# Kernel optimization log

Hardware: AMD Instinct MI355X
Metric: run time of the kernel (lower is better)

The kernel has to match this reference:

```python
import jax, jax.numpy as jnp
import numpy as np

P = 3          # graph partitions
CO = 64        # out_channels
KS = 9         # temporal kernel size (Gamma)
STRIDE = 1     # temporal stride
EPS = 1e-3     # keras BatchNormalization default epsilon


def setup_inputs() -> dict:
    key = jax.random.key(0)
    k1, k2, k3 = jax.random.split(key, 3)
    x = jax.random.normal(k1, (32, 64, 300, 25), dtype=jnp.float32)      # (N, C_in, L, V)
    A = jax.random.uniform(k2, (3, 25, 25), dtype=jnp.float32)           # (P, V, V)
    W = jax.random.normal(k3, (64, 192), dtype=jnp.float32) * 0.05       # (C_in, C_out*P)
    gamma = jnp.ones((64,), dtype=jnp.float32)
    beta = jnp.zeros((64,), dtype=jnp.float32)
    mean = jnp.zeros((64,), dtype=jnp.float32)
    var = jnp.ones((64,), dtype=jnp.float32)
    return {"x": x, "A": A, "W": W, "gamma": gamma, "beta": beta, "mean": mean, "var": var}


def _lt_matrix(L):
    # sum of shifted identities: lt[r, r + i*STRIDE] = 1 for i in [0, KS//STRIDE)
    lt = jnp.zeros((L, L), dtype=jnp.float32)
    for i in range(KS // STRIDE):
        lt = lt + jnp.eye(L, k=i * STRIDE, dtype=jnp.float32)
    return lt


def reference(x, A, W, gamma, beta, mean, var):
    N, C, L, V = x.shape
    res = x  # identity residual (in_channels == out_channels, stride == 1)
    # 1x1 conv: (N,C,L,V) x (C, CO*P) -> (N, CO*P, L, V); channel k = c*P + p (split into CO groups of P)
    y = jnp.einsum('nclv,ck->nklv', x, W)
    y = y.reshape(N, CO, P, L, V)  # (N, C_out, P, L, V)
    # partitioned graph matmul over joints: contract V with A[p]
    z = jnp.einsum('ncplv,pvw->ncplw', y, A)
    # temporal aggregation via handcrafted banded matrix, then sum over partitions
    lt = _lt_matrix(L)
    t = jnp.einsum('ncplv,lm->ncmv', z, lt)  # partition sum fused into einsum
    # BN (inference) over channel axis + ReLU
    inv = gamma / jnp.sqrt(var + EPS)
    xn = (t - mean[None, :, None, None]) * inv[None, :, None, None] + beta[None, :, None, None]
    xn = jax.nn.relu(xn)
    # residual add + final ReLU (dropout is identity at inference)
    return jax.nn.relu(xn + res)
```

## Files before the change

kernel.cpp:

```cpp
#include <hip/hip_runtime.h>
#include <cstdint>
#include <cstddef>

typedef short bf16x8 __attribute__((ext_vector_type(8)));
typedef float f32x4 __attribute__((ext_vector_type(4)));

#define EPS 1e-3f

__device__ __forceinline__ unsigned short f32_to_bf16(float f) {
    union { float f; uint32_t u; } v; v.f = f;
    uint32_t u = v.u;
    return (unsigned short)((u + 0x7FFFu + ((u >> 16) & 1u)) >> 16);
}

__global__ __launch_bounds__(256) void prep_kernel(const float* __restrict__ A,
                                                   const float* __restrict__ W,
                                                   unsigned short* __restrict__ wt,
                                                   unsigned short* __restrict__ at) {
    int idx = blockIdx.x * 256 + threadIdx.x;
    if (idx < 12288) {
        int kp = idx >> 6, ci = idx & 63;
        wt[idx] = f32_to_bf16(W[ci * 192 + kp]);
    } else {
        int j = idx - 12288;
        if (j < 3072) {
            int w = j / 96, k = j - w * 96;
            float val = 0.f;
            if (w < 25 && k < 75) {
                int p = k / 25, v = k - p * 25;
                val = A[(p * 25 + v) * 25 + w];
            }
            at[j] = f32_to_bf16(val);
        }
    }
}

__global__ __launch_bounds__(256) void window_kernel(const float* __restrict__ x,
                                                     unsigned short* __restrict__ xw) {
    int ci = blockIdx.x, n = blockIdx.y;
    __shared__ float sl[7500];
    const float4* xp4 = (const float4*)(x + (size_t)(n * 64 + ci) * 7500);
    float4* sl4 = (float4*)sl;
    for (int i = threadIdx.x; i < 1875; i += 256) sl4[i] = xp4[i];
    __syncthreads();
    unsigned short* base = xw + (size_t)n * 491520 + ci * 256;
    for (int i = threadIdx.x; i < 3840; i += 256) {
        int ch = i >> 7;
        int col = (i & 127) << 1;
        int e0 = ch * 250 + col;
        ushort2 r;
        #pragma unroll
        for (int h = 0; h < 2; ++h) {
            int e = e0 + h;
            float t = 0.f;
            if (e < 7500) {
                int m = e / 25, w = e - m * 25;
                int lo = m - 8 > 0 ? m - 8 : 0;
                for (int l = lo; l <= m; ++l) t += sl[l * 25 + w];
            }
            unsigned short b = f32_to_bf16(t);
            if (h == 0) r.x = b; else r.y = b;
        }
        *(ushort2*)(base + ch * 16384 + col) = r;
    }
}

__global__ __launch_bounds__(256, 2) void fused_kernel(
    const unsigned short* __restrict__ xw, const unsigned short* __restrict__ wt,
    const unsigned short* __restrict__ at, const float* __restrict__ x,
    const float* __restrict__ gamma, const float* __restrict__ beta,
    const float* __restrict__ mean, const float* __restrict__ var,
    float* __restrict__ out) {
    int chunk = blockIdx.x;
    int n = blockIdx.y;
    int l0 = chunk * 10;
    int tid = threadIdx.x;
    int wv = tid >> 6, lane = tid & 63, q = lane >> 4, lcol = lane & 15;

    __shared__ unsigned short Ys[160 * 104];
    __shared__ float scs[64], shs[64];

    if (tid < 64) {
        float sc = gamma[tid] * rsqrtf(var[tid] + EPS);
        scs[tid] = sc;
        shs[tid] = beta[tid] - mean[tid] * sc;
    }
    for (int i = tid; i < 5120; i += 256) {
        int r = i >> 5, j = 72 + (i & 31);
        Ys[r * 104 + j] = 0;
    }

    const unsigned short* xwb = xw + (size_t)n * 491520 + chunk * 16384;
    bf16x8 b1[4][2];
    #pragma unroll
    for (int nt = 0; nt < 4; ++nt) {
        #pragma unroll
        for (int s = 0; s < 2; ++s) {
            const unsigned short* p = xwb + (32 * s + 8 * q) * 256 + wv * 64 + nt * 16 + lcol;
            bf16x8 f;
            #pragma unroll
            for (int j = 0; j < 8; ++j) f[j] = (short)p[j * 256];
            b1[nt][s] = f;
        }
    }
    bf16x8 b2[2][3];
    #pragma unroll
    for (int nt = 0; nt < 2; ++nt)
        #pragma unroll
        for (int s = 0; s < 3; ++s)
            b2[nt][s] = *(const bf16x8*)(at + (nt * 16 + lcol) * 96 + 32 * s + 8 * q);

    for (int g = 0; g < 4; ++g) {
        f32x4 acc[3][4];
        #pragma unroll
        for (int mt = 0; mt < 3; ++mt)
            #pragma unroll
            for (int nt = 0; nt < 4; ++nt) acc[mt][nt] = (f32x4){0.f, 0.f, 0.f, 0.f};
        #pragma unroll
        for (int s = 0; s < 2; ++s) {
            #pragma unroll
            for (int mt = 0; mt < 3; ++mt) {
                bf16x8 a1 = *(const bf16x8*)(wt + (g * 48 + mt * 16 + lcol) * 64 + 32 * s + 8 * q);
                #pragma unroll
                for (int nt = 0; nt < 4; ++nt)
                    acc[mt][nt] = __builtin_amdgcn_mfma_f32_16x16x32_bf16(a1, b1[nt][s], acc[mt][nt], 0, 0, 0);
            }
        }
        __syncthreads();
        #pragma unroll
        for (int mt = 0; mt < 3; ++mt) {
            #pragma unroll
            for (int nt = 0; nt < 4; ++nt) {
                int col = wv * 64 + nt * 16 + lcol;
                if (col < 250) {
                    int ll = col / 25, v = col - ll * 25;
                    int rowbase = ll * 16;
                    #pragma unroll
                    for (int r = 0; r < 4; ++r) {
                        int kp = mt * 16 + 4 * q + r;
                        int cl = kp / 3, p = kp - cl * 3;
                        Ys[(rowbase + cl) * 104 + p * 25 + v] = f32_to_bf16(acc[mt][nt][r]);
                    }
                }
            }
        }
        __syncthreads();
        for (int l = wv; l < 10; l += 4) {
            f32x4 c0 = {0.f, 0.f, 0.f, 0.f}, c1 = {0.f, 0.f, 0.f, 0.f};
            #pragma unroll
            for (int s = 0; s < 3; ++s) {
                bf16x8 a2 = *(const bf16x8*)&Ys[(l * 16 + lcol) * 104 + 32 * s + 8 * q];
                c0 = __builtin_amdgcn_mfma_f32_16x16x32_bf16(a2, b2[0][s], c0, 0, 0, 0);
                c1 = __builtin_amdgcn_mfma_f32_16x16x32_bf16(a2, b2[1][s], c1, 0, 0, 0);
            }
            #pragma unroll
            for (int nt = 0; nt < 2; ++nt) {
                int w = nt * 16 + lcol;
                if (w < 25) {
                    f32x4 cc = nt ? c1 : c0;
                    #pragma unroll
                    for (int r = 0; r < 4; ++r) {
                        int c = g * 16 + 4 * q + r;
                        size_t gi = ((size_t)(n * 64 + c) * 300 + (l0 + l)) * 25 + w;
                        float o = fmaxf(cc[r] * scs[c] + shs[c], 0.f);
                        out[gi] = fmaxf(o + x[gi], 0.f);
                    }
                }
            }
        }
    }
}

extern "C" void kernel_launch(void* const* d_in, const int* in_sizes, int n_in,
                              void* d_out, int out_size, void* d_ws, size_t ws_size,
                              hipStream_t stream) {
    const float* x     = (const float*)d_in[0];
    const float* A     = (const float*)d_in[1];
    const float* W     = (const float*)d_in[2];
    const float* gamma = (const float*)d_in[3];
    const float* beta  = (const float*)d_in[4];
    const float* mean  = (const float*)d_in[5];
    const float* var   = (const float*)d_in[6];
    float* out = (float*)d_out;

    char* ws = (char*)d_ws;
    unsigned short* wt = (unsigned short*)ws;
    unsigned short* at = (unsigned short*)(ws + 24576);
    unsigned short* xw = (unsigned short*)(ws + 30720);

    prep_kernel<<<60, 256, 0, stream>>>(A, W, wt, at);
    window_kernel<<<dim3(64, 32), 256, 0, stream>>>(x, xw);
    fused_kernel<<<dim3(30, 32), 256, 0, stream>>>(xw, wt, at, x, gamma, beta, mean, var, out);
}
```

Before: 186.3 us.

## Fuse temporal window sum into main kernel, removing intermediate bf16 buffer

Removes the separate window kernel and its global bf16 intermediate. Each block now computes the 9-tap sliding temporal sum for its 10-timestep chunk directly from x with a running sum and stages it in shared memory in an MFMA-friendly layout. The block grows to 512 threads, so each wave handles half as many columns. This saves one launch and a global write+read round trip, at the cost of strided uncoalesced reads of x with an 8-step halo overlap per chunk.

```diff
diff --git a/kernel.cpp b/kernel.cpp
--- a/kernel.cpp
+++ b/kernel.cpp
@@ -7,10 +7,10 @@
 
 #define EPS 1e-3f
 
-__device__ __forceinline__ unsigned short f32_to_bf16(float f) {
+__device__ __forceinline__ short f32_to_bf16s(float f) {
     union { float f; uint32_t u; } v; v.f = f;
     uint32_t u = v.u;
-    return (unsigned short)((u + 0x7FFFu + ((u >> 16) & 1u)) >> 16);
+    return (short)((u + 0x7FFFu + ((u >> 16) & 1u)) >> 16);
 }
 
 __global__ __launch_bounds__(256) void prep_kernel(const float* __restrict__ A,
@@ -20,7 +20,7 @@
     int idx = blockIdx.x * 256 + threadIdx.x;
     if (idx < 12288) {
         int kp = idx >> 6, ci = idx & 63;
-        wt[idx] = f32_to_bf16(W[ci * 192 + kp]);
+        wt[idx] = (unsigned short)f32_to_bf16s(W[ci * 192 + kp]);
     } else {
         int j = idx - 12288;
         if (j < 3072) {
@@ -30,54 +30,24 @@
                 int p = k / 25, v = k - p * 25;
                 val = A[(p * 25 + v) * 25 + w];
             }
-            at[j] = f32_to_bf16(val);
+            at[j] = (unsigned short)f32_to_bf16s(val);
         }
     }
 }
 
-__global__ __launch_bounds__(256) void window_kernel(const float* __restrict__ x,
-                                                     unsigned short* __restrict__ xw) {
-    int ci = blockIdx.x, n = blockIdx.y;
-    __shared__ float sl[7500];
-    const float4* xp4 = (const float4*)(x + (size_t)(n * 64 + ci) * 7500);
-    float4* sl4 = (float4*)sl;
-    for (int i = threadIdx.x; i < 1875; i += 256) sl4[i] = xp4[i];
-    __syncthreads();
-    unsigned short* base = xw + (size_t)n * 491520 + ci * 256;
-    for (int i = threadIdx.x; i < 3840; i += 256) {
-        int ch = i >> 7;
-        int col = (i & 127) << 1;
-        int e0 = ch * 250 + col;
-        ushort2 r;
-        #pragma unroll
-        for (int h = 0; h < 2; ++h) {
-            int e = e0 + h;
-            float t = 0.f;
-            if (e < 7500) {
-                int m = e / 25, w = e - m * 25;
-                int lo = m - 8 > 0 ? m - 8 : 0;
-                for (int l = lo; l <= m; ++l) t += sl[l * 25 + w];
-            }
-            unsigned short b = f32_to_bf16(t);
-            if (h == 0) r.x = b; else r.y = b;
-        }
-        *(ushort2*)(base + ch * 16384 + col) = r;
-    }
-}
-
-__global__ __launch_bounds__(256, 2) void fused_kernel(
-    const unsigned short* __restrict__ xw, const unsigned short* __restrict__ wt,
-    const unsigned short* __restrict__ at, const float* __restrict__ x,
+__global__ __launch_bounds__(512, 4) void mega_kernel(
+    const float* __restrict__ x,
+    const unsigned short* __restrict__ wt,
+    const unsigned short* __restrict__ at,
     const float* __restrict__ gamma, const float* __restrict__ beta,
     const float* __restrict__ mean, const float* __restrict__ var,
     float* __restrict__ out) {
-    int chunk = blockIdx.x;
-    int n = blockIdx.y;
-    int l0 = chunk * 10;
+    int ch = blockIdx.x, n = blockIdx.y;
+    int l0 = ch * 10;
     int tid = threadIdx.x;
     int wv = tid >> 6, lane = tid & 63, q = lane >> 4, lcol = lane & 15;
 
-    __shared__ unsigned short Ys[160 * 104];
+    __shared__ short smem[16640];
     __shared__ float scs[64], shs[64];
 
     if (tid < 64) {
@@ -85,71 +55,91 @@
         scs[tid] = sc;
         shs[tid] = beta[tid] - mean[tid] * sc;
     }
-    for (int i = tid; i < 5120; i += 256) {
-        int r = i >> 5, j = 72 + (i & 31);
-        Ys[r * 104 + j] = 0;
+
+    #pragma unroll 1
+    for (int rep = 0; rep < 4; ++rep) {
+        int cidx = tid + rep * 512;
+        if (cidx < 1600) {
+            int ci = cidx / 25, v = cidx - ci * 25;
+            const float* xp = x + (size_t)(n * 64 + ci) * 7500 + v;
+            float vals[18];
+            #pragma unroll
+            for (int i = 0; i < 18; ++i) {
+                int l = l0 - 8 + i;
+                vals[i] = (l >= 0) ? xp[l * 25] : 0.f;
+            }
+            float run = 0.f;
+            #pragma unroll
+            for (int i = 0; i < 8; ++i) run += vals[i];
+            int base = (ci >> 3) * 2056 + (ci & 7);
+            #pragma unroll
+            for (int j = 0; j < 10; ++j) {
+                run += vals[j + 8];
+                smem[base + (j * 25 + v) * 8] = f32_to_bf16s(run);
+                run -= vals[j];
+            }
+        }
     }
+    __syncthreads();
 
-    const unsigned short* xwb = xw + (size_t)n * 491520 + chunk * 16384;
-    bf16x8 b1[4][2];
+    bf16x8 b1[2][2];
     #pragma unroll
-    for (int nt = 0; nt < 4; ++nt) {
+    for (int nt = 0; nt < 2; ++nt)
         #pragma unroll
         for (int s = 0; s < 2; ++s) {
-            const unsigned short* p = xwb + (32 * s + 8 * q) * 256 + wv * 64 + nt * 16 + lcol;
-            bf16x8 f;
-            #pragma unroll
-            for (int j = 0; j < 8; ++j) f[j] = (short)p[j * 256];
-            b1[nt][s] = f;
+            int col = wv * 32 + nt * 16 + lcol;
+            b1[nt][s] = *(const bf16x8*)&smem[(4 * s + q) * 2056 + col * 8];
         }
-    }
     bf16x8 b2[2][3];
     #pragma unroll
     for (int nt = 0; nt < 2; ++nt)
         #pragma unroll
         for (int s = 0; s < 3; ++s)
-            b2[nt][s] = *(const bf16x8*)(at + (nt * 16 + lcol) * 96 + 32 * s + 8 * q);
+            b2[nt][s] = *(const bf16x8*)(at + (size_t)(nt * 16 + lcol) * 96 + 32 * s + 8 * q);
+    __syncthreads();
+
+    for (int i = tid; i < 5120; i += 512) {
+        int r = i >> 5, jj = 72 + (i & 31);
+        smem[r * 104 + jj] = 0;
+    }
 
     for (int g = 0; g < 4; ++g) {
-        f32x4 acc[3][4];
+        f32x4 acc[3][2];
         #pragma unroll
         for (int mt = 0; mt < 3; ++mt)
             #pragma unroll
-            for (int nt = 0; nt < 4; ++nt) acc[mt][nt] = (f32x4){0.f, 0.f, 0.f, 0.f};
+            for (int nt = 0; nt < 2; ++nt) acc[mt][nt] = (f32x4){0.f, 0.f, 0.f, 0.f};
         #pragma unroll
-        for (int s = 0; s < 2; ++s) {
+        for (int s = 0; s < 2; ++s)
             #pragma unroll
             for (int mt = 0; mt < 3; ++mt) {
-                bf16x8 a1 = *(const bf16x8*)(wt + (g * 48 + mt * 16 + lcol) * 64 + 32 * s + 8 * q);
+                bf16x8 a1 = *(const bf16x8*)(wt + (size_t)(g * 48 + mt * 16 + lcol) * 64 + 32 * s + 8 * q);
                 #pragma unroll
-                for (int nt = 0; nt < 4; ++nt)
+                for (int nt = 0; nt < 2; ++nt)
                     acc[mt][nt] = __builtin_amdgcn_mfma_f32_16x16x32_bf16(a1, b1[nt][s], acc[mt][nt], 0, 0, 0);
             }
-        }
         __syncthreads();
         #pragma unroll
-        for (int mt = 0; mt < 3; ++mt) {
+        for (int mt = 0; mt < 3; ++mt)
             #pragma unroll
-            for (int nt = 0; nt < 4; ++nt) {
-                int col = wv * 64 + nt * 16 + lcol;
+            for (int nt = 0; nt < 2; ++nt) {
+                int col = wv * 32 + nt * 16 + lcol;
                 if (col < 250) {
                     int ll = col / 25, v = col - ll * 25;
-                    int rowbase = ll * 16;
                     #pragma unroll
                     for (int r = 0; r < 4; ++r) {
                         int kp = mt * 16 + 4 * q + r;
                         int cl = kp / 3, p = kp - cl * 3;
-                        Ys[(rowbase + cl) * 104 + p * 25 + v] = f32_to_bf16(acc[mt][nt][r]);
+                        smem[(ll * 16 + cl) * 104 + p * 25 + v] = f32_to_bf16s(acc[mt][nt][r]);
                     }
                 }
             }
-        }
         __syncthreads();
-        for (int l = wv; l < 10; l += 4) {
+        for (int l = wv; l < 10; l += 8) {
             f32x4 c0 = {0.f, 0.f, 0.f, 0.f}, c1 = {0.f, 0.f, 0.f, 0.f};
             #pragma unroll
             for (int s = 0; s < 3; ++s) {
-                bf16x8 a2 = *(const bf16x8*)&Ys[(l * 16 + lcol) * 104 + 32 * s + 8 * q];
+                bf16x8 a2 = *(const bf16x8*)&smem[(l * 16 + lcol) * 104 + 32 * s + 8 * q];
                 c0 = __builtin_amdgcn_mfma_f32_16x16x32_bf16(a2, b2[0][s], c0, 0, 0, 0);
                 c1 = __builtin_amdgcn_mfma_f32_16x16x32_bf16(a2, b2[1][s], c1, 0, 0, 0);
             }
@@ -186,9 +176,7 @@
     char* ws = (char*)d_ws;
     unsigned short* wt = (unsigned short*)ws;
     unsigned short* at = (unsigned short*)(ws + 24576);
-    unsigned short* xw = (unsigned short*)(ws + 30720);
 
     prep_kernel<<<60, 256, 0, stream>>>(A, W, wt, at);
-    window_kernel<<<dim3(64, 32), 256, 0, stream>>>(x, xw);
-    fused_kernel<<<dim3(30, 32), 256, 0, stream>>>(xw, wt, at, x, gamma, beta, mean, var, out);
+    mega_kernel<<<dim3(30, 32), 512, 0, stream>>>(x, wt, at, gamma, beta, mean, var, out);
 }
```

Measured after the change: 167.4 us. -10.2%, faster.
